# Performance work log

Hardware: AMD Instinct MI355X
Metric: run time of the kernel (lower is better)

Reference implementation:

```python
import jax, jax.numpy as jnp
import numpy as np

IN_CH, OUT_CH, Z1, B = 794, 512, 1024, 32768


def _build_masks(rng):
    # MADE connectivity masks, same construction as the torch module
    m0 = np.concatenate([np.ones(10, dtype=np.int64), np.arange(1, 785)])  # len 794
    m1 = rng.integers(1, IN_CH, size=Z1)
    m2 = rng.integers(m1.min(), IN_CH, size=OUT_CH)
    MW0 = (m1[:, None] >= m0[None, :IN_CH]).astype(np.float32)  # [Z1, IN_CH]
    MW1 = (m2[:, None] >= m1[None, :]).astype(np.float32)        # [OUT_CH, Z1]
    return jnp.asarray(MW0), jnp.asarray(MW1)


def setup_inputs() -> dict:
    key = jax.random.key(0)
    ks = jax.random.split(key, 9)
    s1 = 1.0 / np.sqrt(IN_CH)
    s2 = 1.0 / np.sqrt(Z1)
    MW0, MW1 = _build_masks(np.random.default_rng(0))
    return {
        "x":   jax.random.normal(ks[0], (B, IN_CH), dtype=jnp.float32),
        "W1":  jax.random.uniform(ks[1], (Z1, IN_CH), jnp.float32, -s1, s1),
        "b1":  jax.random.uniform(ks[2], (Z1,), jnp.float32, -s1, s1),
        "Wc1": jax.random.uniform(ks[3], (Z1, IN_CH), jnp.float32, -s1, s1),
        "bc1": jax.random.uniform(ks[4], (Z1,), jnp.float32, -s1, s1),
        "W2":  jax.random.uniform(ks[5], (OUT_CH, Z1), jnp.float32, -s2, s2),
        "b2":  jax.random.uniform(ks[6], (OUT_CH,), jnp.float32, -s2, s2),
        "Wc2": jax.random.uniform(ks[7], (OUT_CH, Z1), jnp.float32, -s2, s2),
        "bc2": jax.random.uniform(ks[8], (OUT_CH,), jnp.float32, -s2, s2),
        "MW0": MW0,
        "MW1": MW1,
    }


def reference(x, W1, b1, Wc1, bc1, W2, b2, Wc2, bc2, MW0, MW1):
    # F.linear(ones_like(x), Wc, bc) == row-sum of masked Wc + bc (same math, no GEMM)
    mW1, mWc1 = W1 * MW0, Wc1 * MW0
    h1 = jax.nn.relu(x @ mW1.T + b1 + jnp.sum(mWc1, axis=1) + bc1)  # [B, Z1]
    mW2, mWc2 = W2 * MW1, Wc2 * MW1
    h2 = jax.nn.relu(h1 @ mW2.T + b2 + jnp.sum(mWc2, axis=1) + bc2)  # [B, OUT_CH]
    return h2
```

## Files before the change

### kernel.cpp

```cpp
#include <hip/hip_runtime.h>
#include <hip/hip_bf16.h>
#include <stdint.h>

#define IN_CH 794
#define KPAD  832
#define Z1C   1024
#define OUT_C 512
#define BATCH 32768

typedef __attribute__((ext_vector_type(8))) short short8;
typedef __attribute__((ext_vector_type(4))) float f32x4;

__device__ __forceinline__ ushort f2bf(float f) {
  uint32_t u = __float_as_uint(f);
  return (ushort)((u + 0x7fffu + ((u >> 16) & 1u)) >> 16);
}

__device__ __forceinline__ void glds16(const void* g, void* l) {
  __builtin_amdgcn_global_load_lds(
      (const __attribute__((address_space(1))) void*)g,
      (__attribute__((address_space(3))) void*)l, 16, 0, 0);
}

#define BAR() __builtin_amdgcn_s_barrier()
#define MFMA(a, b, c) __builtin_amdgcn_mfma_f32_16x16x32_bf16(a, b, c, 0, 0, 0)

__global__ __launch_bounds__(256) void prep1(
    const float* __restrict__ W1, const float* __restrict__ b1,
    const float* __restrict__ Wc1, const float* __restrict__ bc1,
    const float* __restrict__ MW0, ushort* __restrict__ w1p,
    float* __restrict__ bias1) {
  int z = blockIdx.x, t = threadIdx.x;
  float sum = 0.f;
  for (int i = t; i < KPAD; i += 256) {
    float w = 0.f;
    if (i < IN_CH) {
      float m = MW0[z * IN_CH + i];
      w = W1[z * IN_CH + i] * m;
      sum += Wc1[z * IN_CH + i] * m;
    }
    w1p[z * KPAD + i] = f2bf(w);
  }
#pragma unroll
  for (int o = 32; o > 0; o >>= 1) sum += __shfl_down(sum, o, 64);
  __shared__ float red[4];
  if ((t & 63) == 0) red[t >> 6] = sum;
  __syncthreads();
  if (t == 0) bias1[z] = b1[z] + bc1[z] + red[0] + red[1] + red[2] + red[3];
}

__global__ __launch_bounds__(256) void prep2(
    const float* __restrict__ W2, const float* __restrict__ b2,
    const float* __restrict__ Wc2, const float* __restrict__ bc2,
    const float* __restrict__ MW1, ushort* __restrict__ w2m,
    float* __restrict__ bias2) {
  int z = blockIdx.x, t = threadIdx.x;
  float sum = 0.f;
  for (int i = t; i < Z1C; i += 256) {
    float m = MW1[z * Z1C + i];
    w2m[z * Z1C + i] = f2bf(W2[z * Z1C + i] * m);
    sum += Wc2[z * Z1C + i] * m;
  }
#pragma unroll
  for (int o = 32; o > 0; o >>= 1) sum += __shfl_down(sum, o, 64);
  __shared__ float red[4];
  if ((t & 63) == 0) red[t >> 6] = sum;
  __syncthreads();
  if (t == 0) bias2[z] = b2[z] + bc2[z] + red[0] + red[1] + red[2] + red[3];
}

__global__ __launch_bounds__(256) void xcvt(const float* __restrict__ x,
                                            ushort* __restrict__ xb) {
  const int CPR = KPAD / 8;
  const int total = BATCH * CPR;
  for (int i = blockIdx.x * 256 + threadIdx.x; i < total;
       i += gridDim.x * 256) {
    int row = i / CPR;
    int col = (i - row * CPR) * 8;
    const float* p = x + (size_t)row * IN_CH + col;
    ushort u[8];
    if (col + 8 <= IN_CH) {
#pragma unroll
      for (int j = 0; j < 4; ++j) {
        float2 v = *(const float2*)(p + j * 2);
        u[j * 2] = f2bf(v.x);
        u[j * 2 + 1] = f2bf(v.y);
      }
    } else {
#pragma unroll
      for (int j = 0; j < 8; ++j) u[j] = (col + j < IN_CH) ? f2bf(p[j]) : 0;
    }
    *(uint4*)(xb + (size_t)row * KPAD + col) = *(uint4*)u;
  }
}

template <int KP, int NKT, int NCB, int OSTR, bool BF16OUT>
__global__ __launch_bounds__(512, 2) void gemmT(
    const ushort* __restrict__ Ag, const ushort* __restrict__ Bg,
    const float* __restrict__ bias, void* __restrict__ Cout) {
  __shared__ uint4 ldsq[10240];
  char* const L = (char*)ldsq;
  char* const LB = L + 98304;
  const int tid = threadIdx.x;
  const int lane = tid & 63, wid = tid >> 6;
  const int wr = wid >> 2, wc = wid & 3;

  const int nwg = gridDim.x;
  const int w0 = blockIdx.x;
  const int swz = (w0 & 7) * (nwg >> 3) + (w0 >> 3);
  const int bcol = (swz % NCB) * 256;
  const int brow = (swz / NCB) * 256;

  const int srow = tid >> 3;
  const int scol = ((tid & 7) * 16) ^ ((srow & 7) << 4);
  const char* gAp = (const char*)Ag + (size_t)(brow + srow) * (KP * 2) + scol;
  const char* gBp = (const char*)Bg + (size_t)(bcol + srow) * (KP * 2) + scol;
  const int ldst = wid * 1024;

  auto stA = [&](int buf, int kt, int h) {
    glds16(gAp + (size_t)h * (64 * KP * 2) + (size_t)kt * 128,
           L + buf * 32768 + h * 8192 + ldst);
  };
  auto stB = [&](int buf, int kt, int h) {
    glds16(gBp + (size_t)h * (64 * KP * 2) + (size_t)kt * 128,
           LB + buf * 32768 + h * 8192 + ldst);
  };

  const int rA = lane & 15;
  const int klo = (lane >> 4) * 16;
  const int xs = (rA & 7) << 4;
  auto rdA = [&](const char* Ab, int m, int ks) -> short8 {
    int row = wr * 128 + m * 16 + rA;
    return *(const short8*)(Ab + row * 128 + ((ks * 64 + klo) ^ xs));
  };
  auto rdB = [&](const char* Bb, int n, int ks) -> short8 {
    int row = wc * 64 + n * 16 + rA;
    return *(const short8*)(Bb + row * 128 + ((ks * 64 + klo) ^ xs));
  };

  f32x4 acc[8][4] = {};

#pragma unroll
  for (int h = 0; h < 4; ++h) stA(0, 0, h);
#pragma unroll
  for (int h = 0; h < 4; ++h) stB(0, 0, h);
#pragma unroll
  for (int h = 0; h < 4; ++h) stA(1, 1, h);
  asm volatile("s_waitcnt vmcnt(4)" ::: "memory");
  BAR();

  for (int j = 0; j < NKT; ++j) {
    const char* Ab = L + (j % 3) * 32768;
    const char* Bb = LB + (j & 1) * 32768;
    const int jn = j + 1, ja = j + 2;
    const int bb1 = jn & 1, ab2 = ja % 3;
    short8 aF[4][2], bF[4][2];

#pragma unroll
    for (int m = 0; m < 4; ++m) {
      aF[m][0] = rdA(Ab, m, 0); aF[m][1] = rdA(Ab, m, 1);
    }
#pragma unroll
    for (int n = 0; n < 2; ++n) {
      bF[n][0] = rdB(Bb, n, 0); bF[n][1] = rdB(Bb, n, 1);
    }
    if (jn < NKT) { stB(bb1, jn, 0); stB(bb1, jn, 1); }
    BAR();
    __builtin_amdgcn_s_setprio(1);
#pragma unroll
    for (int ks = 0; ks < 2; ++ks)
#pragma unroll
      for (int m = 0; m < 4; ++m)
#pragma unroll
        for (int n = 0; n < 2; ++n)
          acc[m][n] = MFMA(aF[m][ks], bF[n][ks], acc[m][n]);
    __builtin_amdgcn_s_setprio(0);
    BAR();

#pragma unroll
    for (int n = 2; n < 4; ++n) {
      bF[n][0] = rdB(Bb, n, 0); bF[n][1] = rdB(Bb, n, 1);
    }
    if (jn < NKT) { stB(bb1, jn, 2); stB(bb1, jn, 3); }
    BAR();
    __builtin_amdgcn_s_setprio(1);
#pragma unroll
    for (int ks = 0; ks < 2; ++ks)
#pragma unroll
      for (int m = 0; m < 4; ++m)
#pragma unroll
        for (int n = 2; n < 4; ++n)
          acc[m][n] = MFMA(aF[m][ks], bF[n][ks], acc[m][n]);
    __builtin_amdgcn_s_setprio(0);
    BAR();

#pragma unroll
    for (int m = 0; m < 4; ++m) {
      aF[m][0] = rdA(Ab, m + 4, 0); aF[m][1] = rdA(Ab, m + 4, 1);
    }
    if (ja < NKT) { stA(ab2, ja, 0); stA(ab2, ja, 1); }
    BAR();
    __builtin_amdgcn_s_setprio(1);
#pragma unroll
    for (int ks = 0; ks < 2; ++ks)
#pragma unroll
      for (int m = 0; m < 4; ++m)
#pragma unroll
        for (int n = 0; n < 2; ++n)
          acc[m + 4][n] = MFMA(aF[m][ks], bF[n][ks], acc[m + 4][n]);
    __builtin_amdgcn_s_setprio(0);
    BAR();

    if (ja < NKT) { stA(ab2, ja, 2); stA(ab2, ja, 3); }
    BAR();
    __builtin_amdgcn_s_setprio(1);
#pragma unroll
    for (int ks = 0; ks < 2; ++ks)
#pragma unroll
      for (int m = 0; m < 4; ++m)
#pragma unroll
        for (int n = 2; n < 4; ++n)
          acc[m + 4][n] = MFMA(aF[m][ks], bF[n][ks], acc[m + 4][n]);
    __builtin_amdgcn_s_setprio(0);
    if (ja < NKT)
      asm volatile("s_waitcnt vmcnt(4)" ::: "memory");
    else if (jn < NKT)
      asm volatile("s_waitcnt vmcnt(0)" ::: "memory");
    BAR();
  }

  if (BF16OUT) {
    char* const LT = (char*)ldsq;
#pragma unroll
    for (int h = 0; h < 2; ++h) {
      if (wr == h) {
#pragma unroll
        for (int n = 0; n < 4; ++n) {
          const int col = wc * 64 + n * 16 + rA;
          const float bv = bias[bcol + col];
#pragma unroll
          for (int m = 0; m < 8; ++m)
#pragma unroll
            for (int r = 0; r < 4; ++r) {
              const int R = m * 16 + (lane >> 4) * 4 + r;
              float v = acc[m][n][r] + bv;
              v = v > 0.f ? v : 0.f;
              *(ushort*)(LT + R * 512 + ((col * 2) ^ ((R & 7) << 4))) = f2bf(v);
            }
        }
      }
      __syncthreads();
#pragma unroll
      for (int it = 0; it < 8; ++it) {
        const int idx = it * 8192 + tid * 16;
        const int R = idx >> 9, cb = idx & 511;
        uint4 v = *(const uint4*)(LT + R * 512 + (cb ^ ((R & 7) << 4)));
        *(uint4*)((char*)Cout + (size_t)(brow + h * 128 + R) * (OSTR * 2) +
                  bcol * 2 + cb) = v;
      }
      if (h == 0) __syncthreads();
    }
  } else {
#pragma unroll
    for (int n = 0; n < 4; ++n) {
      const int col = bcol + wc * 64 + n * 16 + rA;
      const float bv = bias[col];
#pragma unroll
      for (int m = 0; m < 8; ++m) {
#pragma unroll
        for (int r = 0; r < 4; ++r) {
          const int row = brow + wr * 128 + m * 16 + (lane >> 4) * 4 + r;
          float v = acc[m][n][r] + bv;
          v = v > 0.f ? v : 0.f;
          ((float*)Cout)[(size_t)row * OSTR + col] = v;
        }
      }
    }
  }
}

__global__ __launch_bounds__(256, 2) void gemm1_fused(
    const float* __restrict__ x, const ushort* __restrict__ w1p,
    const float* __restrict__ bias1, ushort* __restrict__ h1) {
  __shared__ ushort As[128 * 32];
  __shared__ ushort Bs[128 * 32];
  const int tid = threadIdx.x;
  const int lane = tid & 63, wid = tid >> 6;
  const int wr = wid >> 1, wc = wid & 1;
  const int brow = blockIdx.x * 128;
  const int bcol = blockIdx.y * 128;
  f32x4 acc[4][4] = {};
  const int arow = tid >> 1;
  const int acol0 = (tid & 1) * 16;
  const float* xrow = x + (size_t)(brow + arow) * IN_CH;
  for (int kt = 0; kt < 26; ++kt) {
    const int k0 = kt * 32;
#pragma unroll
    for (int c = 0; c < 2; ++c) {
      int idx16 = (wid * 2 + c) * 64 + lane;
      int row = idx16 >> 2, chunk = idx16 & 3;
      glds16(w1p + (size_t)(bcol + row) * KPAD + k0 + chunk * 8,
             (char*)Bs + (wid * 2 + c) * 1024);
    }
    union { ushort u[16]; uint4 q[2]; } pk;
    if (kt < 24) {
      const float* p = xrow + k0 + acol0;
#pragma unroll
      for (int j = 0; j < 8; ++j) {
        float2 v = *(const float2*)(p + j * 2);
        pk.u[j * 2] = f2bf(v.x);
        pk.u[j * 2 + 1] = f2bf(v.y);
      }
    } else {
#pragma unroll
      for (int j = 0; j < 16; ++j) {
        int col = k0 + acol0 + j;
        pk.u[j] = f2bf(col < IN_CH ? xrow[col] : 0.f);
      }
    }
    *(uint4*)&As[arow * 32 + acol0] = pk.q[0];
    *(uint4*)&As[arow * 32 + acol0 + 8] = pk.q[1];
    __syncthreads();
    const int kb = (lane >> 4) * 8, rA = lane & 15;
    short8 af[4], bfrag[4];
#pragma unroll
    for (int m = 0; m < 4; ++m)
      af[m] = *(const short8*)&As[(wr * 64 + m * 16 + rA) * 32 + kb];
#pragma unroll
    for (int n = 0; n < 4; ++n)
      bfrag[n] = *(const short8*)&Bs[(wc * 64 + n * 16 + rA) * 32 + kb];
#pragma unroll
    for (int m = 0; m < 4; ++m)
#pragma unroll
      for (int n = 0; n < 4; ++n)
        acc[m][n] = MFMA(af[m], bfrag[n], acc[m][n]);
    __syncthreads();
  }
  const int orow0 = brow + wr * 64;
  const int ocol0 = bcol + wc * 64;
#pragma unroll
  for (int n = 0; n < 4; ++n) {
    int col = ocol0 + n * 16 + (lane & 15);
    float bv = bias1[col];
#pragma unroll
    for (int m = 0; m < 4; ++m)
#pragma unroll
      for (int r = 0; r < 4; ++r) {
        int row = orow0 + m * 16 + (lane >> 4) * 4 + r;
        float v = acc[m][n][r] + bv;
        v = v > 0.f ? v : 0.f;
        h1[(size_t)row * Z1C + col] = f2bf(v);
      }
  }
}

extern "C" void kernel_launch(void* const* d_in, const int* in_sizes, int n_in,
                              void* d_out, int out_size, void* d_ws, size_t ws_size,
                              hipStream_t stream) {
  (void)in_sizes; (void)n_in; (void)out_size;
  const float* x   = (const float*)d_in[0];
  const float* W1  = (const float*)d_in[1];
  const float* b1  = (const float*)d_in[2];
  const float* Wc1 = (const float*)d_in[3];
  const float* bc1 = (const float*)d_in[4];
  const float* W2  = (const float*)d_in[5];
  const float* b2  = (const float*)d_in[6];
  const float* Wc2 = (const float*)d_in[7];
  const float* bc2 = (const float*)d_in[8];
  const float* MW0 = (const float*)d_in[9];
  const float* MW1 = (const float*)d_in[10];

  char* ws = (char*)d_ws;
  ushort* w1p   = (ushort*)ws;
  ushort* w2m   = (ushort*)(ws + 1703936);
  float*  bias1 = (float*)(ws + 2752512);
  float*  bias2 = (float*)(ws + 2756608);
  ushort* xb    = (ushort*)(ws + 2758656);
  const size_t WS_NEED = 2758656ull + 54525952ull;

  ushort* h1 = (ushort*)d_out;
  float*  out = (float*)d_out;

  prep1<<<1024, 256, 0, stream>>>(W1, b1, Wc1, bc1, MW0, w1p, bias1);
  prep2<<<512, 256, 0, stream>>>(W2, b2, Wc2, bc2, MW1, w2m, bias2);

  if (ws_size >= WS_NEED) {
    xcvt<<<2048, 256, 0, stream>>>(x, xb);
    gemmT<KPAD, 13, 4, Z1C, true><<<512, 512, 0, stream>>>(xb, w1p, bias1, h1);
  } else {
    gemm1_fused<<<dim3(256, 8), 256, 0, stream>>>(x, w1p, bias1, h1);
  }
  gemmT<Z1C, 16, 2, OUT_C, false><<<256, 512, 0, stream>>>(h1, w2m, bias2, out);
}
```

Measured before the change: 134.8 us.

## Merge weight prep kernels and make GEMM1 tiles persistent over two column blocks

Combines the two weight-masking prep kernels into one launch to save a launch. GEMM1 becomes a dedicated kernel with 256 workgroups, each computing two adjacent 256-column output tiles. The A tiles and the first B tile for the second pass are prefetched into LDS while the first tile's epilogue runs. The epilogue is split into 64-row chunks staged through a separate LDS region. This halves the grid and adds more sequential work per block, so it may lose parallelism or occupancy.

```diff
diff --git a/kernel.cpp b/kernel.cpp
--- a/kernel.cpp
+++ b/kernel.cpp
@@ -25,48 +25,46 @@
 #define BAR() __builtin_amdgcn_s_barrier()
 #define MFMA(a, b, c) __builtin_amdgcn_mfma_f32_16x16x32_bf16(a, b, c, 0, 0, 0)
 
-__global__ __launch_bounds__(256) void prep1(
+__global__ __launch_bounds__(256) void prepM(
     const float* __restrict__ W1, const float* __restrict__ b1,
     const float* __restrict__ Wc1, const float* __restrict__ bc1,
     const float* __restrict__ MW0, ushort* __restrict__ w1p,
-    float* __restrict__ bias1) {
-  int z = blockIdx.x, t = threadIdx.x;
+    float* __restrict__ bias1, const float* __restrict__ W2,
+    const float* __restrict__ b2, const float* __restrict__ Wc2,
+    const float* __restrict__ bc2, const float* __restrict__ MW1,
+    ushort* __restrict__ w2m, float* __restrict__ bias2) {
+  const int t = threadIdx.x;
+  __shared__ float red[4];
   float sum = 0.f;
-  for (int i = t; i < KPAD; i += 256) {
-    float w = 0.f;
-    if (i < IN_CH) {
-      float m = MW0[z * IN_CH + i];
-      w = W1[z * IN_CH + i] * m;
-      sum += Wc1[z * IN_CH + i] * m;
-    }
-    w1p[z * KPAD + i] = f2bf(w);
-  }
-#pragma unroll
-  for (int o = 32; o > 0; o >>= 1) sum += __shfl_down(sum, o, 64);
-  __shared__ float red[4];
-  if ((t & 63) == 0) red[t >> 6] = sum;
-  __syncthreads();
-  if (t == 0) bias1[z] = b1[z] + bc1[z] + red[0] + red[1] + red[2] + red[3];
-}
-
-__global__ __launch_bounds__(256) void prep2(
-    const float* __restrict__ W2, const float* __restrict__ b2,
-    const float* __restrict__ Wc2, const float* __restrict__ bc2,
-    const float* __restrict__ MW1, ushort* __restrict__ w2m,
-    float* __restrict__ bias2) {
-  int z = blockIdx.x, t = threadIdx.x;
-  float sum = 0.f;
-  for (int i = t; i < Z1C; i += 256) {
-    float m = MW1[z * Z1C + i];
-    w2m[z * Z1C + i] = f2bf(W2[z * Z1C + i] * m);
-    sum += Wc2[z * Z1C + i] * m;
-  }
-#pragma unroll
-  for (int o = 32; o > 0; o >>= 1) sum += __shfl_down(sum, o, 64);
-  __shared__ float red[4];
-  if ((t & 63) == 0) red[t >> 6] = sum;
-  __syncthreads();
-  if (t == 0) bias2[z] = b2[z] + bc2[z] + red[0] + red[1] + red[2] + red[3];
+  if (blockIdx.x < 1024) {
+    const int z = blockIdx.x;
+    for (int i = t; i < KPAD; i += 256) {
+      float w = 0.f;
+      if (i < IN_CH) {
+        float m = MW0[z * IN_CH + i];
+        w = W1[z * IN_CH + i] * m;
+        sum += Wc1[z * IN_CH + i] * m;
+      }
+      w1p[z * KPAD + i] = f2bf(w);
+    }
+#pragma unroll
+    for (int o = 32; o > 0; o >>= 1) sum += __shfl_down(sum, o, 64);
+    if ((t & 63) == 0) red[t >> 6] = sum;
+    __syncthreads();
+    if (t == 0) bias1[z] = b1[z] + bc1[z] + red[0] + red[1] + red[2] + red[3];
+  } else {
+    const int z = blockIdx.x - 1024;
+    for (int i = t; i < Z1C; i += 256) {
+      float m = MW1[z * Z1C + i];
+      w2m[z * Z1C + i] = f2bf(W2[z * Z1C + i] * m);
+      sum += Wc2[z * Z1C + i] * m;
+    }
+#pragma unroll
+    for (int o = 32; o > 0; o >>= 1) sum += __shfl_down(sum, o, 64);
+    if ((t & 63) == 0) red[t >> 6] = sum;
+    __syncthreads();
+    if (t == 0) bias2[z] = b2[z] + bc2[z] + red[0] + red[1] + red[2] + red[3];
+  }
 }
 
 __global__ __launch_bounds__(256) void xcvt(const float* __restrict__ x,
@@ -94,10 +92,203 @@
   }
 }
 
-template <int KP, int NKT, int NCB, int OSTR, bool BF16OUT>
+__global__ __launch_bounds__(512, 2) void gemm1_k(
+    const ushort* __restrict__ Ag, const ushort* __restrict__ Bg,
+    const float* __restrict__ bias, ushort* __restrict__ h1) {
+  __shared__ uint4 ldsq[10240];
+  char* const L = (char*)ldsq;
+  char* const LB = L + 98304;
+  char* const LT = L + 65536;
+  const int tid = threadIdx.x;
+  const int lane = tid & 63, wid = tid >> 6;
+  const int wr = wid >> 2, wc = wid & 3;
+
+  const int nwg = gridDim.x;
+  const int w0 = blockIdx.x;
+  const int swz = (w0 & 7) * (nwg >> 3) + (w0 >> 3);
+  const int pair = swz & 1;
+  const int brow = (swz >> 1) * 256;
+
+  const int srow = tid >> 3;
+  const int scol = ((tid & 7) * 16) ^ ((srow & 7) << 4);
+  const char* gAp = (const char*)Ag + (size_t)(brow + srow) * 1664 + scol;
+  const int ldst = wid * 1024;
+
+  const int rA = lane & 15;
+  const int klo = (lane >> 4) * 16;
+  const int xs = (rA & 7) << 4;
+
+  auto stA = [&](int buf, int kt, int h) {
+    glds16(gAp + (size_t)h * (64 * 1664) + (size_t)kt * 128,
+           L + buf * 32768 + h * 8192 + ldst);
+  };
+  auto rdA = [&](const char* Ab, int m, int ks) -> short8 {
+    int row = wr * 128 + m * 16 + rA;
+    return *(const short8*)(Ab + row * 128 + ((ks * 64 + klo) ^ xs));
+  };
+  auto rdB = [&](const char* Bb, int n, int ks) -> short8 {
+    int row = wc * 64 + n * 16 + rA;
+    return *(const short8*)(Bb + row * 128 + ((ks * 64 + klo) ^ xs));
+  };
+
+#pragma unroll 1
+  for (int c2 = 0; c2 < 2; ++c2) {
+    const int bcol = pair * 512 + c2 * 256;
+    const char* gBp = (const char*)Bg + (size_t)(bcol + srow) * 1664 + scol;
+    auto stB = [&](int buf, int kt, int h) {
+      glds16(gBp + (size_t)h * (64 * 1664) + (size_t)kt * 128,
+             LB + buf * 32768 + h * 8192 + ldst);
+    };
+
+    if (c2 == 0) {
+#pragma unroll
+      for (int h = 0; h < 4; ++h) stA(0, 0, h);
+#pragma unroll
+      for (int h = 0; h < 4; ++h) stB(0, 0, h);
+#pragma unroll
+      for (int h = 0; h < 4; ++h) stA(1, 1, h);
+      asm volatile("s_waitcnt vmcnt(4)" ::: "memory");
+      BAR();
+    }
+
+    f32x4 acc[8][4] = {};
+
+    for (int j = 0; j < 13; ++j) {
+      const char* Ab = L + (j % 3) * 32768;
+      const char* Bb = LB + (j & 1) * 32768;
+      const int jn = j + 1, ja = j + 2;
+      const int bb1 = jn & 1, ab2 = ja % 3;
+      short8 aF[4][2], bF[4][2];
+
+#pragma unroll
+      for (int m = 0; m < 4; ++m) {
+        aF[m][0] = rdA(Ab, m, 0); aF[m][1] = rdA(Ab, m, 1);
+      }
+#pragma unroll
+      for (int n = 0; n < 2; ++n) {
+        bF[n][0] = rdB(Bb, n, 0); bF[n][1] = rdB(Bb, n, 1);
+      }
+      if (jn < 13) { stB(bb1, jn, 0); stB(bb1, jn, 1); }
+      BAR();
+      __builtin_amdgcn_s_setprio(1);
+#pragma unroll
+      for (int ks = 0; ks < 2; ++ks)
+#pragma unroll
+        for (int m = 0; m < 4; ++m)
+#pragma unroll
+          for (int n = 0; n < 2; ++n)
+            acc[m][n] = MFMA(aF[m][ks], bF[n][ks], acc[m][n]);
+      __builtin_amdgcn_s_setprio(0);
+      BAR();
+
+#pragma unroll
+      for (int n = 2; n < 4; ++n) {
+        bF[n][0] = rdB(Bb, n, 0); bF[n][1] = rdB(Bb, n, 1);
+      }
+      if (jn < 13) { stB(bb1, jn, 2); stB(bb1, jn, 3); }
+      BAR();
+      __builtin_amdgcn_s_setprio(1);
+#pragma unroll
+      for (int ks = 0; ks < 2; ++ks)
+#pragma unroll
+        for (int m = 0; m < 4; ++m)
+#pragma unroll
+          for (int n = 2; n < 4; ++n)
+            acc[m][n] = MFMA(aF[m][ks], bF[n][ks], acc[m][n]);
+      __builtin_amdgcn_s_setprio(0);
+      BAR();
+
+#pragma unroll
+      for (int m = 0; m < 4; ++m) {
+        aF[m][0] = rdA(Ab, m + 4, 0); aF[m][1] = rdA(Ab, m + 4, 1);
+      }
+      if (ja < 13) { stA(ab2, ja, 0); stA(ab2, ja, 1); }
+      BAR();
+      __builtin_amdgcn_s_setprio(1);
+#pragma unroll
+      for (int ks = 0; ks < 2; ++ks)
+#pragma unroll
+        for (int m = 0; m < 4; ++m)
+#pragma unroll
+          for (int n = 0; n < 2; ++n)
+            acc[m + 4][n] = MFMA(aF[m][ks], bF[n][ks], acc[m + 4][n]);
+      __builtin_amdgcn_s_setprio(0);
+      BAR();
+
+      if (ja < 13) { stA(ab2, ja, 2); stA(ab2, ja, 3); }
+      BAR();
+      __builtin_amdgcn_s_setprio(1);
+#pragma unroll
+      for (int ks = 0; ks < 2; ++ks)
+#pragma unroll
+        for (int m = 0; m < 4; ++m)
+#pragma unroll
+          for (int n = 2; n < 4; ++n)
+            acc[m + 4][n] = MFMA(aF[m][ks], bF[n][ks], acc[m + 4][n]);
+      __builtin_amdgcn_s_setprio(0);
+      if (ja < 13)
+        asm volatile("s_waitcnt vmcnt(4)" ::: "memory");
+      else if (jn < 13)
+        asm volatile("s_waitcnt vmcnt(0)" ::: "memory");
+      BAR();
+    }
+
+    if (c2 == 0) {
+      const int bcol1 = pair * 512 + 256;
+      const char* gBp1 = (const char*)Bg + (size_t)(bcol1 + srow) * 1664 + scol;
+#pragma unroll
+      for (int h = 0; h < 4; ++h) stA(0, 0, h);
+#pragma unroll
+      for (int h = 0; h < 4; ++h) stA(1, 1, h);
+#pragma unroll
+      for (int h = 0; h < 4; ++h)
+        glds16(gBp1 + (size_t)h * (64 * 1664), LB + h * 8192 + ldst);
+    }
+
+#pragma unroll
+    for (int q = 0; q < 4; ++q) {
+      if (wr == (q >> 1)) {
+#pragma unroll
+        for (int n = 0; n < 4; ++n) {
+          const int col = wc * 64 + n * 16 + rA;
+          const float bv = bias[bcol + col];
+#pragma unroll
+          for (int mi = 0; mi < 4; ++mi) {
+            const int m = (q & 1) * 4 + mi;
+#pragma unroll
+            for (int r = 0; r < 4; ++r) {
+              const int R = mi * 16 + (lane >> 4) * 4 + r;
+              float v = acc[m][n][r] + bv;
+              v = v > 0.f ? v : 0.f;
+              *(ushort*)(LT + R * 512 + ((col * 2) ^ ((R & 7) << 4))) = f2bf(v);
+            }
+          }
+        }
+      }
+      __syncthreads();
+#pragma unroll
+      for (int it = 0; it < 4; ++it) {
+        const int idx = it * 8192 + tid * 16;
+        const int R = idx >> 9, cb = idx & 511;
+        uint4 v = *(const uint4*)(LT + R * 512 + (cb ^ ((R & 7) << 4)));
+        *(uint4*)((char*)h1 + (size_t)(brow + q * 64 + R) * 2048 + bcol * 2 +
+                  cb) = v;
+      }
+      __syncthreads();
+    }
+
+    if (c2 == 0) {
+      asm volatile("s_waitcnt vmcnt(16)" ::: "memory");
+      asm volatile("s_waitcnt lgkmcnt(0)" ::: "memory");
+      BAR();
+    }
+  }
+}
+
+template <int KP, int NKT, int NCB, int OSTR>
 __global__ __launch_bounds__(512, 2) void gemmT(
     const ushort* __restrict__ Ag, const ushort* __restrict__ Bg,
-    const float* __restrict__ bias, void* __restrict__ Cout) {
+    const float* __restrict__ bias, float* __restrict__ Cout) {
   __shared__ uint4 ldsq[10240];
   char* const L = (char*)ldsq;
   char* const LB = L + 98304;
@@ -229,51 +420,18 @@
     BAR();
   }
 
-  if (BF16OUT) {
-    char* const LT = (char*)ldsq;
-#pragma unroll
-    for (int h = 0; h < 2; ++h) {
-      if (wr == h) {
-#pragma unroll
-        for (int n = 0; n < 4; ++n) {
-          const int col = wc * 64 + n * 16 + rA;
-          const float bv = bias[bcol + col];
-#pragma unroll
-          for (int m = 0; m < 8; ++m)
-#pragma unroll
-            for (int r = 0; r < 4; ++r) {
-              const int R = m * 16 + (lane >> 4) * 4 + r;
-              float v = acc[m][n][r] + bv;
-              v = v > 0.f ? v : 0.f;
-              *(ushort*)(LT + R * 512 + ((col * 2) ^ ((R & 7) << 4))) = f2bf(v);
-            }
-        }
-      }
-      __syncthreads();
-#pragma unroll
-      for (int it = 0; it < 8; ++it) {
-        const int idx = it * 8192 + tid * 16;
-        const int R = idx >> 9, cb = idx & 511;
-        uint4 v = *(const uint4*)(LT + R * 512 + (cb ^ ((R & 7) << 4)));
-        *(uint4*)((char*)Cout + (size_t)(brow + h * 128 + R) * (OSTR * 2) +
-                  bcol * 2 + cb) = v;
-      }
-      if (h == 0) __syncthreads();
-    }
-  } else {
-#pragma unroll
-    for (int n = 0; n < 4; ++n) {
-      const int col = bcol + wc * 64 + n * 16 + rA;
-      const float bv = bias[col];
-#pragma unroll
-      for (int m = 0; m < 8; ++m) {
-#pragma unroll
-        for (int r = 0; r < 4; ++r) {
-          const int row = brow + wr * 128 + m * 16 + (lane >> 4) * 4 + r;
-          float v = acc[m][n][r] + bv;
-          v = v > 0.f ? v : 0.f;
-          ((float*)Cout)[(size_t)row * OSTR + col] = v;
-        }
+#pragma unroll
+  for (int n = 0; n < 4; ++n) {
+    const int col = bcol + wc * 64 + n * 16 + rA;
+    const float bv = bias[col];
+#pragma unroll
+    for (int m = 0; m < 8; ++m) {
+#pragma unroll
+      for (int r = 0; r < 4; ++r) {
+        const int row = brow + wr * 128 + m * 16 + (lane >> 4) * 4 + r;
+        float v = acc[m][n][r] + bv;
+        v = v > 0.f ? v : 0.f;
+        Cout[(size_t)row * OSTR + col] = v;
       }
     }
   }
@@ -381,14 +539,14 @@
   ushort* h1 = (ushort*)d_out;
   float*  out = (float*)d_out;
 
-  prep1<<<1024, 256, 0, stream>>>(W1, b1, Wc1, bc1, MW0, w1p, bias1);
-  prep2<<<512, 256, 0, stream>>>(W2, b2, Wc2, bc2, MW1, w2m, bias2);
+  prepM<<<1536, 256, 0, stream>>>(W1, b1, Wc1, bc1, MW0, w1p, bias1,
+                                  W2, b2, Wc2, bc2, MW1, w2m, bias2);
 
   if (ws_size >= WS_NEED) {
     xcvt<<<2048, 256, 0, stream>>>(x, xb);
-    gemmT<KPAD, 13, 4, Z1C, true><<<512, 512, 0, stream>>>(xb, w1p, bias1, h1);
+    gemm1_k<<<256, 512, 0, stream>>>(xb, w1p, bias1, h1);
   } else {
     gemm1_fused<<<dim3(256, 8), 256, 0, stream>>>(x, w1p, bias1, h1);
   }
-  gemmT<Z1C, 16, 2, OUT_C, false><<<256, 512, 0, stream>>>(h1, w2m, bias2, out);
-}
+  gemmT<Z1C, 16, 2, OUT_C><<<256, 512, 0, stream>>>(h1, w2m, bias2, out);
+}
```

Measured after the change: 162.8 us. +20.7%, slower.
